# Performance work log

Measured on AMD Instinct MI355X. Metric: run time of the kernel, lower is better.

## Reference

```python
import jax, jax.numpy as jnp
import numpy as np

Q, B, D = 512, 4, 1024      # qlen, batch, d_model
L, H, DH, DI = 4, 16, 64, 4096  # layers, heads, d_head, d_inner
M = 512                      # mem_len


def setup_inputs() -> dict:
    key = jax.random.key(0)
    ks = jax.random.split(key, 10)
    w = lambda i, shape: jax.random.normal(ks[i], shape, jnp.float32) * 0.02
    return dict(
        x=jax.random.normal(ks[0], (Q, B, D), jnp.float32),
        mems=jax.random.normal(ks[1], (L, M, B, D), jnp.float32),
        u=w(2, (H, DH)),
        v=w(3, (H, DH)),
        W_qkv=w(4, (L, D, 3 * H * DH)),
        W_o=w(5, (L, H * DH, D)),
        W_r=w(6, (L, D, H * DH)),
        ln1_g=jnp.ones((L, D), jnp.float32),
        ln1_b=jnp.zeros((L, D), jnp.float32),
        W1=w(7, (L, D, DI)),
        b1=jnp.zeros((L, DI), jnp.float32),
        W2=w(8, (L, DI, D)),
        b2=jnp.zeros((L, D), jnp.float32),
        ln2_g=jnp.ones((L, D), jnp.float32),
        ln2_b=jnp.zeros((L, D), jnp.float32),
    )


def _layer_norm(x, g, b):
    mu = x.mean(-1, keepdims=True)
    var = ((x - mu) ** 2).mean(-1, keepdims=True)
    return (x - mu) * jax.lax.rsqrt(var + 1e-5) * g + b


def _rel_shift(x):
    # x: [q, k, b, n] -> Transformer-XL relative shift
    q, k, b, n = x.shape
    x = jnp.pad(x, ((0, 0), (1, 0), (0, 0), (0, 0)))
    return x.reshape(k + 1, q, b, n)[1:].reshape(q, k, b, n)


def _pos_emb(klen, d):
    pos = jnp.arange(klen - 1, -1, -1.0, dtype=jnp.float32)
    inv_freq = 1.0 / (10000.0 ** (jnp.arange(0, d, 2, dtype=jnp.float32) / d))
    ang = pos[:, None] * inv_freq[None, :]
    return jnp.concatenate([jnp.sin(ang), jnp.cos(ang)], axis=-1)  # [klen, d]


def reference(x, mems, u, v, W_qkv, W_o, W_r, ln1_g, ln1_b, W1, b1, W2, b2, ln2_g, ln2_b):
    q_len, bsz, d = x.shape
    mlen = mems.shape[1]
    klen = mlen + q_len
    r = _pos_emb(klen, d)                       # [klen, d]
    scale = 1.0 / np.sqrt(DH)
    # causal mask with memory: query i may attend key j iff j - i <= mlen
    mask = (jnp.arange(klen)[None, :] - jnp.arange(q_len)[:, None]) > mlen  # [q, k]
    h = x
    for i in range(L):
        cat = jnp.concatenate([mems[i], h], axis=0)       # [klen, b, d]
        heads = cat @ W_qkv[i]                            # [klen, b, 3*H*DH]
        qh, kh, vh = jnp.split(heads, 3, axis=-1)
        qh = qh[-q_len:].reshape(q_len, bsz, H, DH)
        kh = kh.reshape(klen, bsz, H, DH)
        vh = vh.reshape(klen, bsz, H, DH)
        rk = (r @ W_r[i]).reshape(klen, H, DH)            # [klen, H, DH]
        AC = jnp.einsum('ibnd,jbnd->ijbn', qh + u, kh)
        BD = _rel_shift(jnp.einsum('ibnd,jnd->ijbn', qh + v, rk))
        score = (AC + BD) * scale                         # [q, k, b, n]
        score = jnp.where(mask[:, :, None, None], -1e30, score)
        attn = jax.nn.softmax(score, axis=1)
        av = jnp.einsum('ijbn,jbnd->ibnd', attn, vh).reshape(q_len, bsz, H * DH)
        h = _layer_norm(h + av @ W_o[i], ln1_g[i], ln1_b[i])
        ff = jax.nn.relu(h @ W1[i] + b1[i]) @ W2[i] + b2[i]
        h = _layer_norm(h + ff, ln2_g[i], ln2_b[i])
    return h  # [qlen, bsz, d_model]
```

## Files before the change

kernel.cpp:

```cpp
#include <hip/hip_runtime.h>
#include <hip/hip_bf16.h>
#include <cstdint>

#define QL      512
#define BS      4
#define DMODEL  1024
#define NL      4
#define NH      16
#define DHEAD   64
#define DINNER  4096
#define MLEN    512
#define KLEN_   1024
#define HD_     1024
#define THD     3072
#define ROWS_H   2048

typedef __attribute__((ext_vector_type(8))) __bf16 bf16x8;
typedef __attribute__((ext_vector_type(4))) __bf16 bf16x4;
typedef __attribute__((ext_vector_type(4))) float  f32x4;

enum EpiMode { EPI_F32 = 0, EPI_BF16 = 1, EPI_RELU_BF16 = 2 };

__device__ __forceinline__ void glds16(const void* g, void* l) {
  __builtin_amdgcn_global_load_lds(
      (const __attribute__((address_space(1))) unsigned int*)g,
      (__attribute__((address_space(3))) unsigned int*)l, 16, 0, 0);
}

template<int BM, int BN, int WMT, int WNT, int EPI>
__global__ __launch_bounds__(256) void gemm_bt(
    const __bf16* __restrict__ A, const __bf16* __restrict__ Bt,
    void* __restrict__ Cv, const float* __restrict__ bias,
    int K, int lda, int ldb, int ldc,
    long sA, long Bn, long Cn)
{
  constexpr int WCOLS = BN / (WNT * 16);
  constexpr int WROWS = BM / (WMT * 16);
  static_assert(WCOLS * WROWS == 4, "must be 4 waves");
  __shared__ __align__(16) char smem[(BM + BN) * 64];
  char* sAm = smem;
  char* sBm = smem + BM * 64;

  const int bz = blockIdx.z;
  A  += (size_t)bz * sA;
  Bt += (size_t)bz * Bn;
  const size_t coff = (size_t)bz * Cn;

  const int tid  = threadIdx.x;
  const int wave = tid >> 6, lane = tid & 63;
  const int quad = lane >> 4, mrow = lane & 15;
  const int wr = wave / WCOLS, wc = wave % WCOLS;
  const int bm0 = blockIdx.x * BM, bn0 = blockIdx.y * BN;

  const int srow = lane >> 2;
  const int skq  = (lane & 3) ^ (srow & 3);
  const __bf16* gA = A  + (size_t)(bm0 + wave * (BM / 64) * 16 + srow) * lda + skq * 8;
  const __bf16* gB = Bt + (size_t)(bn0 + wave * (BN / 64) * 16 + srow) * ldb + skq * 8;
  char* lA = sAm + wave * (BM / 64) * 1024;
  char* lB = sBm + wave * (BN / 64) * 1024;

  const int aswz = (quad ^ (mrow & 3)) << 4;

  const f32x4 zero = {0.f, 0.f, 0.f, 0.f};
  f32x4 acc[WMT][WNT];
#pragma unroll
  for (int a = 0; a < WMT; ++a)
#pragma unroll
    for (int b = 0; b < WNT; ++b) acc[a][b] = zero;

  for (int k0 = 0; k0 < K; k0 += 32) {
#pragma unroll
    for (int p = 0; p < BM / 64; ++p)
      glds16(gA + (size_t)p * 16 * lda + k0, lA + p * 1024);
#pragma unroll
    for (int p = 0; p < BN / 64; ++p)
      glds16(gB + (size_t)p * 16 * ldb + k0, lB + p * 1024);
    __syncthreads();
    bf16x8 afr[WMT], bfr[WNT];
#pragma unroll
    for (int mt = 0; mt < WMT; ++mt)
      afr[mt] = *(const bf16x8*)(sAm + (wr * (WMT * 16) + mt * 16 + mrow) * 64 + aswz);
#pragma unroll
    for (int nt = 0; nt < WNT; ++nt)
      bfr[nt] = *(const bf16x8*)(sBm + (wc * (WNT * 16) + nt * 16 + mrow) * 64 + aswz);
#pragma unroll
    for (int mt = 0; mt < WMT; ++mt)
#pragma unroll
      for (int nt = 0; nt < WNT; ++nt)
        acc[mt][nt] = __builtin_amdgcn_mfma_f32_16x16x32_bf16(afr[mt], bfr[nt], acc[mt][nt], 0, 0, 0);
    __syncthreads();
  }

#pragma unroll
  for (int mt = 0; mt < WMT; ++mt) {
#pragma unroll
    for (int nt = 0; nt < WNT; ++nt) {
#pragma unroll
      for (int rr = 0; rr < 4; ++rr) {
        int gm = bm0 + wr * (WMT * 16) + mt * 16 + quad * 4 + rr;
        int gn = bn0 + wc * (WNT * 16) + nt * 16 + mrow;
        float val = acc[mt][nt][rr];
        if constexpr (EPI == EPI_F32) {
          ((float*)Cv)[coff + (size_t)gm * ldc + gn] = val;
        } else if constexpr (EPI == EPI_BF16) {
          ((__bf16*)Cv)[coff + (size_t)gm * ldc + gn] = (__bf16)val;
        } else {
          val += bias[gn];
          ((__bf16*)Cv)[coff + (size_t)gm * ldc + gn] = (__bf16)fmaxf(val, 0.f);
        }
      }
    }
  }
}

__global__ __launch_bounds__(256) void flash_attn(
    const __bf16* __restrict__ qu,
    const __bf16* __restrict__ qv,
    const __bf16* __restrict__ heads,
    const __bf16* __restrict__ rk,
    const __bf16* __restrict__ vt,
    __bf16* __restrict__ avp,
    float* __restrict__ mlpart)
{
  __shared__ __align__(16) char kh_t[64 * 144];
  __shared__ __align__(16) char rv_t[64 * 144];
  __shared__ float raw[64 * 132];

  const int wgid = blockIdx.x;
  const int xcd  = wgid & 7;
  const int slotw = wgid >> 3;
  const int bn   = ((slotw >> 4) << 3) + xcd;
  const int inner = slotw & 15;
  const int t    = inner & 7;
  const int z    = inner >> 3;
  const int i0   = t * 64;
  const int b    = bn >> 4, n = bn & 15;
  const int nt   = t + 9;
  const int h    = (nt + 1) >> 1;
  const int ks   = z ? h : 0;
  const int ke   = z ? nt : h;

  const int tid = threadIdx.x;
  const int wave = tid >> 6, lane = tid & 63;
  const int quad = lane >> 4, mrow = lane & 15;
  const f32x4 zero = {0.f, 0.f, 0.f, 0.f};

  const __bf16* qub = qu + (size_t)bn * QL * DHEAD;
  const __bf16* qvb = qv + (size_t)bn * QL * DHEAD;
  const int qrow = i0 + wave * 16 + mrow;
  bf16x8 quf0 = *(const bf16x8*)(qub + (size_t)qrow * 64 + quad * 8);
  bf16x8 quf1 = *(const bf16x8*)(qub + (size_t)qrow * 64 + 32 + quad * 8);
  bf16x8 qvf0 = *(const bf16x8*)(qvb + (size_t)qrow * 64 + quad * 8);
  bf16x8 qvf1 = *(const bf16x8*)(qvb + (size_t)qrow * 64 + 32 + quad * 8);

  f32x4 o[4];
#pragma unroll
  for (int dt = 0; dt < 4; ++dt) o[dt] = zero;
  float m_r[4], l_r[4];
#pragma unroll
  for (int rr = 0; rr < 4; ++rr) { m_r[rr] = -3.0e38f; l_r[rr] = 0.f; }

  const int sr = tid >> 3;
  const int sc = (tid & 7) * 8;

  const int c0 = 448 - i0;
  const int cpre = c0 + 64 * ks;
#pragma unroll
  for (int p = 0; p < 2; ++p) {
    int r = p * 32 + sr;
    bf16x8 vv = *(const bf16x8*)(rk + (size_t)(cpre + r) * HD_ + n * 64 + sc);
    *(bf16x8*)(rv_t + r * 144 + sc * 2) = vv;
  }
  __syncthreads();
  {
    int slotc = ((cpre >> 6) & 1) * 64;
    __builtin_amdgcn_s_setprio(1);
#pragma unroll
    for (int ct = 0; ct < 4; ++ct) {
      bf16x8 b0 = *(const bf16x8*)(rv_t + (ct * 16 + mrow) * 144 + quad * 16);
      bf16x8 b1 = *(const bf16x8*)(rv_t + (ct * 16 + mrow) * 144 + 64 + quad * 16);
      f32x4 r = __builtin_amdgcn_mfma_f32_16x16x32_bf16(qvf0, b0, zero, 0, 0, 0);
      r = __builtin_amdgcn_mfma_f32_16x16x32_bf16(qvf1, b1, r, 0, 0, 0);
#pragma unroll
      for (int rr = 0; rr < 4; ++rr)
        raw[(wave * 16 + quad * 4 + rr) * 132 + slotc + ct * 16 + mrow] = r[rr];
    }
    __builtin_amdgcn_s_setprio(0);
  }
  __syncthreads();

  const int i_base = i0 + wave * 16 + quad * 4;
  for (int k = ks; k < ke; ++k) {
    const int j0 = k * 64;
#pragma unroll
    for (int p = 0; p < 2; ++p) {
      int r = p * 32 + sr;
      bf16x8 kv = *(const bf16x8*)(heads + (size_t)((j0 + r) * BS + b) * THD + HD_ + n * 64 + sc);
      *(bf16x8*)(kh_t + r * 144 + sc * 2) = kv;
    }
    const int c0n = c0 + 64 * (k + 1);
    if (c0n < KLEN_) {
#pragma unroll
      for (int p = 0; p < 2; ++p) {
        int r = p * 32 + sr;
        bf16x8 rv = *(const bf16x8*)(rk + (size_t)(c0n + r) * HD_ + n * 64 + sc);
        *(bf16x8*)(rv_t + r * 144 + sc * 2) = rv;
      }
    }
    __syncthreads();
    __builtin_amdgcn_s_setprio(1);
    if (c0n < KLEN_) {
      int slotc = ((c0n >> 6) & 1) * 64;
#pragma unroll
      for (int ct = 0; ct < 4; ++ct) {
        bf16x8 b0 = *(const bf16x8*)(rv_t + (ct * 16 + mrow) * 144 + quad * 16);
        bf16x8 b1 = *(const bf16x8*)(rv_t + (ct * 16 + mrow) * 144 + 64 + quad * 16);
        f32x4 r = __builtin_amdgcn_mfma_f32_16x16x32_bf16(qvf0, b0, zero, 0, 0, 0);
        r = __builtin_amdgcn_mfma_f32_16x16x32_bf16(qvf1, b1, r, 0, 0, 0);
#pragma unroll
        for (int rr = 0; rr < 4; ++rr)
          raw[(wave * 16 + quad * 4 + rr) * 132 + slotc + ct * 16 + mrow] = r[rr];
      }
    }
    f32x4 s[4];
#pragma unroll
    for (int ct = 0; ct < 4; ++ct) {
      bf16x8 b0 = *(const bf16x8*)(kh_t + (ct * 16 + mrow) * 144 + quad * 16);
      bf16x8 b1 = *(const bf16x8*)(kh_t + (ct * 16 + mrow) * 144 + 64 + quad * 16);
      s[ct] = __builtin_amdgcn_mfma_f32_16x16x32_bf16(quf0, b0, zero, 0, 0, 0);
      s[ct] = __builtin_amdgcn_mfma_f32_16x16x32_bf16(quf1, b1, s[ct], 0, 0, 0);
    }
    __builtin_amdgcn_s_setprio(0);
    __syncthreads();
#pragma unroll
    for (int p = 0; p < 2; ++p) {
      int r = p * 32 + sr;
      bf16x8 vv = *(const bf16x8*)(vt + (size_t)bn * (DHEAD * KLEN_) + (size_t)r * KLEN_ + j0 + sc);
      *(bf16x8*)(rv_t + r * 144 + sc * 2) = vv;
    }
#pragma unroll
    for (int ct = 0; ct < 4; ++ct) {
#pragma unroll
      for (int rr = 0; rr < 4; ++rr) {
        int i = i_base + rr;
        int j = j0 + ct * 16 + mrow;
        float val;
        if (j - i <= MLEN) {
          int c = j - i + (QL - 1);
          int col = ((c >> 6) & 1) * 64 + (c & 63);
          val = (s[ct][rr] + raw[(wave * 16 + quad * 4 + rr) * 132 + col]) * 0.125f;
        } else val = -3.0e38f;
        s[ct][rr] = val;
      }
    }
    float alpha[4];
#pragma unroll
    for (int rr = 0; rr < 4; ++rr) {
      float mx = fmaxf(fmaxf(s[0][rr], s[1][rr]), fmaxf(s[2][rr], s[3][rr]));
#pragma unroll
      for (int off = 1; off < 16; off <<= 1) mx = fmaxf(mx, __shfl_xor(mx, off));
      float m_new = fmaxf(m_r[rr], mx);
      alpha[rr] = __expf(m_r[rr] - m_new);
      m_r[rr] = m_new;
      float rs = 0.f;
#pragma unroll
      for (int ct = 0; ct < 4; ++ct) {
        float pv = __expf(s[ct][rr] - m_new);
        s[ct][rr] = pv;
        rs += pv;
      }
#pragma unroll
      for (int off = 1; off < 16; off <<= 1) rs += __shfl_xor(rs, off);
      l_r[rr] = l_r[rr] * alpha[rr] + rs;
    }
#pragma unroll
    for (int dt = 0; dt < 4; ++dt)
#pragma unroll
      for (int rr = 0; rr < 4; ++rr) o[dt][rr] *= alpha[rr];
#pragma unroll
    for (int ct = 0; ct < 4; ++ct)
#pragma unroll
      for (int rr = 0; rr < 4; ++rr)
        ((__bf16*)kh_t)[(wave * 16 + quad * 4 + rr) * 72 + ct * 16 + mrow] = (__bf16)s[ct][rr];
    __syncthreads();
    {
      bf16x8 pf0 = *(const bf16x8*)(kh_t + (wave * 16 + mrow) * 144 + quad * 16);
      bf16x8 pf1 = *(const bf16x8*)(kh_t + (wave * 16 + mrow) * 144 + 64 + quad * 16);
      __builtin_amdgcn_s_setprio(1);
#pragma unroll
      for (int dt = 0; dt < 4; ++dt) {
        bf16x8 vf0 = *(const bf16x8*)(rv_t + (dt * 16 + mrow) * 144 + quad * 16);
        bf16x8 vf1 = *(const bf16x8*)(rv_t + (dt * 16 + mrow) * 144 + 64 + quad * 16);
        o[dt] = __builtin_amdgcn_mfma_f32_16x16x32_bf16(pf0, vf0, o[dt], 0, 0, 0);
        o[dt] = __builtin_amdgcn_mfma_f32_16x16x32_bf16(pf1, vf1, o[dt], 0, 0, 0);
      }
      __builtin_amdgcn_s_setprio(0);
    }
    __syncthreads();
  }

  const size_t prow = ((size_t)z * 64 + bn) * 512;
#pragma unroll
  for (int rr = 0; rr < 4; ++rr) {
    int i = i_base + rr;
    float inv = 1.0f / l_r[rr];
#pragma unroll
    for (int dt = 0; dt < 4; ++dt)
      avp[(prow + i) * 64 + dt * 16 + mrow] = (__bf16)(o[dt][rr] * inv);
  }
  if (mrow == 0) {
#pragma unroll
    for (int rr = 0; rr < 4; ++rr) {
      int i = i_base + rr;
      mlpart[(prow + i) * 2]     = m_r[rr];
      mlpart[(prow + i) * 2 + 1] = l_r[rr];
    }
  }
}

__global__ __launch_bounds__(256) void attn_combine(
    const __bf16* __restrict__ avp, const float* __restrict__ mlpart,
    __bf16* __restrict__ av)
{
  int idx = blockIdx.x * 256 + threadIdx.x;
  int dq = idx & 15;
  int i  = (idx >> 4) & 511;
  int bn = idx >> 13;
  int b = bn >> 4, n = bn & 15;
  size_t r0 = (size_t)bn * 512 + i;
  size_t r1 = r0 + (size_t)64 * 512;
  float m1 = mlpart[r0 * 2], l1 = mlpart[r0 * 2 + 1];
  float m2 = mlpart[r1 * 2], l2 = mlpart[r1 * 2 + 1];
  float m  = fmaxf(m1, m2);
  float w1 = l1 * __expf(m1 - m), w2 = l2 * __expf(m2 - m);
  float inv = 1.0f / (w1 + w2);
  w1 *= inv; w2 *= inv;
  bf16x4 o1 = *(const bf16x4*)(avp + r0 * 64 + dq * 4);
  bf16x4 o2 = *(const bf16x4*)(avp + r1 * 64 + dq * 4);
  bf16x4 ov;
#pragma unroll
  for (int j = 0; j < 4; ++j)
    ov[j] = (__bf16)((float)o1[j] * w1 + (float)o2[j] * w2);
  *(bf16x4*)(av + ((size_t)i * BS + b) * HD_ + n * 64 + dq * 4) = ov;
}


__global__ __launch_bounds__(256) void transpose_f32_bf16(
    const float* __restrict__ in, unsigned short* __restrict__ out, int R, int C)
{
  __shared__ float tile[64][66];
  int c0 = blockIdx.x * 64, r0 = blockIdx.y * 64;
  int tx = threadIdx.x, ty = threadIdx.y;
#pragma unroll
  for (int s = 0; s < 8; ++s) {
    int r = ty + s * 8;
    const float* p = in + (size_t)(r0 + r) * C + c0 + 2 * tx;
    tile[r][2 * tx]     = p[0];
    tile[r][2 * tx + 1] = p[1];
  }
  __syncthreads();
#pragma unroll
  for (int s = 0; s < 8; ++s) {
    int c = ty + s * 8;
    __bf16 lo = (__bf16)tile[2 * tx][c];
    __bf16 hi = (__bf16)tile[2 * tx + 1][c];
    unsigned int w = (unsigned int)*(unsigned short*)&lo |
                     ((unsigned int)*(unsigned short*)&hi << 16);
    *(unsigned int*)(out + (size_t)(c0 + c) * R + r0 + 2 * tx) = w;
  }
}

__global__ __launch_bounds__(256) void cast_f32_bf16(const float* __restrict__ in,
                                                     __bf16* __restrict__ out, int n)
{
  int i = blockIdx.x * 256 + threadIdx.x;
  if (i < n) out[i] = (__bf16)in[i];
}

__global__ __launch_bounds__(256) void posemb_kernel(__bf16* __restrict__ r)
{
  int idx = blockIdx.x * 256 + threadIdx.x;
  int p = idx >> 10, c = idx & 1023;
  int t = c & 511;
  float invf = __expf(-((float)t / 512.0f) * 9.210340371976184f);
  float ang = (float)(KLEN_ - 1 - p) * invf;
  float val = (c < 512) ? sinf(ang) : cosf(ang);
  r[idx] = (__bf16)val;
}

__global__ __launch_bounds__(256) void init_h(const float* __restrict__ x,
                                              float* __restrict__ hm,
                                              __bf16* __restrict__ hbf, int n)
{
  int i = blockIdx.x * 256 + threadIdx.x;
  if (i < n) { float t = x[i]; hm[i] = t; hbf[i] = (__bf16)t; }
}

__global__ __launch_bounds__(256) void build_quqv(const __bf16* __restrict__ heads,
                                                  const float* __restrict__ u,
                                                  const float* __restrict__ v,
                                                  __bf16* __restrict__ qu,
                                                  __bf16* __restrict__ qv)
{
  int idx = blockIdx.x * 256 + threadIdx.x;
  int d = idx & 63;
  int i = (idx >> 6) & (QL - 1);
  int bn = idx >> 15;
  int b = bn >> 4, n = bn & 15;
  float q = (float)heads[(size_t)((MLEN + i) * BS + b) * THD + n * 64 + d];
  int ud = n * 64 + d;
  qu[idx] = (__bf16)(q + u[ud]);
  qv[idx] = (__bf16)(q + v[ud]);
}

__global__ __launch_bounds__(256) void build_vt(const unsigned short* __restrict__ heads,
                                                unsigned short* __restrict__ vt)
{
  __shared__ unsigned short tile[64][65];
  int bn = blockIdx.y; int b = bn >> 4, n = bn & 15;
  int j0 = blockIdx.x * 64;
  int tx = threadIdx.x, ty = threadIdx.y;
#pragma unroll
  for (int s = 0; s < 16; ++s) {
    int j = ty + s * 4;
    tile[j][tx] = heads[(size_t)((j0 + j) * BS + b) * THD + 2048 + n * 64 + tx];
  }
  __syncthreads();
#pragma unroll
  for (int s = 0; s < 16; ++s) {
    int d = ty + s * 4;
    vt[(size_t)bn * DHEAD * KLEN_ + (size_t)d * KLEN_ + j0 + tx] = tile[tx][d];
  }
}

__global__ __launch_bounds__(256) void ln_kernel(float* __restrict__ hm,
                                                 const float* __restrict__ d0,
                                                 const float* __restrict__ d1,
                                                 const float* __restrict__ bias,
                                                 const float* __restrict__ g,
                                                 const float* __restrict__ b,
                                                 __bf16* __restrict__ hbf,
                                                 float* __restrict__ outf)
{
  int row = blockIdx.x;
  size_t base = (size_t)row * DMODEL;
  int tid = threadIdx.x;
  float x[4]; float sum = 0.f, sq = 0.f;
#pragma unroll
  for (int p = 0; p < 4; ++p) {
    int c = p * 256 + tid;
    float t = hm[base + c] + d0[base + c];
    if (d1) t += d1[base + c];
    if (bias) t += bias[c];
    x[p] = t; sum += t; sq += t * t;
  }
#pragma unroll
  for (int off = 32; off > 0; off >>= 1) { sum += __shfl_xor(sum, off); sq += __shfl_xor(sq, off); }
  __shared__ float rs[4], rq[4];
  int wave = tid >> 6, lane = tid & 63;
  if (lane == 0) { rs[wave] = sum; rq[wave] = sq; }
  __syncthreads();
  sum = rs[0] + rs[1] + rs[2] + rs[3];
  sq  = rq[0] + rq[1] + rq[2] + rq[3];
  float mu  = sum * (1.0f / DMODEL);
  float var = sq * (1.0f / DMODEL) - mu * mu;
  float rstd = rsqrtf(var + 1e-5f);
#pragma unroll
  for (int p = 0; p < 4; ++p) {
    int c = p * 256 + tid;
    float y = (x[p] - mu) * rstd * g[c] + b[c];
    hm[base + c] = y;
    hbf[base + c] = (__bf16)y;
    if (outf) outf[base + c] = y;
  }
}

extern "C" void kernel_launch(void* const* d_in, const int* in_sizes, int n_in,
                              void* d_out, int out_size, void* d_ws, size_t ws_size,
                              hipStream_t stream) {
  (void)in_sizes; (void)n_in; (void)out_size; (void)ws_size;
  const float* x    = (const float*)d_in[0];
  const float* mems = (const float*)d_in[1];
  const float* u    = (const float*)d_in[2];
  const float* v    = (const float*)d_in[3];
  const float* Wqkv = (const float*)d_in[4];
  const float* Wo   = (const float*)d_in[5];
  const float* Wr   = (const float*)d_in[6];
  const float* ln1g = (const float*)d_in[7];
  const float* ln1b = (const float*)d_in[8];
  const float* W1   = (const float*)d_in[9];
  const float* b1   = (const float*)d_in[10];
  const float* W2   = (const float*)d_in[11];
  const float* b2   = (const float*)d_in[12];
  const float* ln2g = (const float*)d_in[13];
  const float* ln2b = (const float*)d_in[14];

  size_t off = 0;
  char* ws = (char*)d_ws;
  auto alloc = [&](size_t bytes) { size_t o = off; off += (bytes + 255) & ~(size_t)255; return o; };
  __bf16* wT    = (__bf16*)(ws + alloc((size_t)DINNER * DMODEL * 2));
  char*   R1    = (char*)(ws + alloc((size_t)(2 * ROWS_H) * THD * 2));
  __bf16* heads = (__bf16*)R1;
  float*  proj  = (float*)R1;
  __bf16* ff1   = (__bf16*)(R1 + (size_t)ROWS_H * DMODEL * 4);
  __bf16* catb  = (__bf16*)(ws + alloc((size_t)(2 * ROWS_H) * DMODEL * 2));
  __bf16* memsb = catb;
  __bf16* hbf   = catb + (size_t)ROWS_H * DMODEL;
  __bf16* av    = catb;
  float*  mlprt = (float*)hbf;
  __bf16* avp   = wT;
  __bf16* r_bf  = (__bf16*)(ws + alloc((size_t)KLEN_ * DMODEL * 2));
  __bf16* rk4   = (__bf16*)(ws + alloc((size_t)NL * KLEN_ * HD_ * 2));
  __bf16* qu    = (__bf16*)(ws + alloc((size_t)2 * BS * NH * QL * DHEAD * 2));
  __bf16* qv    = qu + (size_t)BS * NH * QL * DHEAD;
  float*  ff2p  = (float*)qu;
  __bf16* vt    = (__bf16*)(ws + alloc((size_t)BS * NH * DHEAD * KLEN_ * 2));
  float*  hm    = (float*)(ws + alloc((size_t)ROWS_H * DMODEL * 4));

  posemb_kernel<<<(KLEN_ * DMODEL) / 256, 256, 0, stream>>>(r_bf);
  init_h<<<(ROWS_H * DMODEL) / 256, 256, 0, stream>>>(x, hm, hbf, ROWS_H * DMODEL);

  for (int i = 0; i < NL; ++i)
    transpose_f32_bf16<<<dim3(HD_ / 64, DMODEL / 64), dim3(32, 8), 0, stream>>>(
        Wr + (size_t)i * DMODEL * HD_, (unsigned short*)(wT + (size_t)i * HD_ * DMODEL),
        DMODEL, HD_);
  gemm_bt<128, 128, 4, 4, EPI_BF16><<<dim3(8, 8, NL), 256, 0, stream>>>(
      r_bf, wT, rk4, nullptr, DMODEL, DMODEL, DMODEL, HD_,
      0, (long)HD_ * DMODEL, (long)KLEN_ * HD_);

  for (int i = 0; i < NL; ++i) {
    cast_f32_bf16<<<(MLEN * BS * DMODEL) / 256, 256, 0, stream>>>(
        mems + (size_t)i * MLEN * BS * DMODEL, memsb, MLEN * BS * DMODEL);
    transpose_f32_bf16<<<dim3(THD / 64, DMODEL / 64), dim3(32, 8), 0, stream>>>(
        Wqkv + (size_t)i * DMODEL * THD, (unsigned short*)wT, DMODEL, THD);
    gemm_bt<128, 128, 4, 4, EPI_BF16><<<dim3(32, 24, 1), 256, 0, stream>>>(
        catb, wT, heads, nullptr, DMODEL, DMODEL, DMODEL, THD, 0, 0, 0);

    build_quqv<<<(BS * NH * QL * DHEAD) / 256, 256, 0, stream>>>(heads, u, v, qu, qv);
    build_vt<<<dim3(KLEN_ / 64, BS * NH), dim3(64, 4), 0, stream>>>(
        (const unsigned short*)heads, (unsigned short*)vt);

    flash_attn<<<dim3(1024), 256, 0, stream>>>(
        qu, qv, heads, rk4 + (size_t)i * KLEN_ * HD_, vt, avp, mlprt);
    attn_combine<<<(64 * 512 * 16) / 256, 256, 0, stream>>>(avp, mlprt, av);

    transpose_f32_bf16<<<dim3(DMODEL / 64, HD_ / 64), dim3(32, 8), 0, stream>>>(
        Wo + (size_t)i * HD_ * DMODEL, (unsigned short*)wT, HD_, DMODEL);
    gemm_bt<128, 64, 4, 2, EPI_F32><<<dim3(16, 16, 1), 256, 0, stream>>>(
        av, wT, proj, nullptr, HD_, HD_, HD_, DMODEL, 0, 0, 0);
    ln_kernel<<<ROWS_H, 256, 0, stream>>>(hm, proj, nullptr, nullptr,
                                          ln1g + i * DMODEL, ln1b + i * DMODEL, hbf, nullptr);

    transpose_f32_bf16<<<dim3(DINNER / 64, DMODEL / 64), dim3(32, 8), 0, stream>>>(
        W1 + (size_t)i * DMODEL * DINNER, (unsigned short*)wT, DMODEL, DINNER);
    gemm_bt<128, 128, 4, 4, EPI_RELU_BF16><<<dim3(16, 32, 1), 256, 0, stream>>>(
        hbf, wT, ff1, b1 + i * DINNER, DMODEL, DMODEL, DMODEL, DINNER, 0, 0, 0);

    transpose_f32_bf16<<<dim3(DMODEL / 64, DINNER / 64), dim3(32, 8), 0, stream>>>(
        W2 + (size_t)i * DINNER * DMODEL, (unsigned short*)wT, DINNER, DMODEL);
    gemm_bt<128, 64, 4, 2, EPI_F32><<<dim3(16, 16, 2), 256, 0, stream>>>(
        ff1, wT, proj, nullptr, DINNER / 2, DINNER, DINNER, DMODEL,
        (long)(DINNER / 2), (long)(DINNER / 2), (long)(ff2p - proj));
    ln_kernel<<<ROWS_H, 256, 0, stream>>>(hm, proj, ff2p, b2 + i * DMODEL,
                                          ln2g + i * DMODEL, ln2b + i * DMODEL, hbf,
                                          (i == NL - 1) ? (float*)d_out : nullptr);
  }
}
```

Before: 1.228 ms.

## Prefetch K/R/V tiles into registers and use exp2 softmax in flash attention

The flash attention loop now loads the next iteration's K and R tiles and the current V tile into registers ahead of time, then writes them to LDS after the barriers. Global load latency should overlap with the MFMA and softmax work instead of stalling before each sync. Softmax moves to base-2 by folding log2(e) into the score scale and using exp2f, including in the combine kernel. The tile-to-workgroup order is reversed so the longer query tiles are scheduled first. In exchange, register pressure rises and occupancy may drop.

```diff
diff --git a/kernel.cpp b/kernel.cpp
--- a/kernel.cpp
+++ b/kernel.cpp
@@ -1,6 +1,7 @@
 #include <hip/hip_runtime.h>
 #include <hip/hip_bf16.h>
 #include <cstdint>
+#include <cmath>
 
 #define QL      512
 #define BS      4
@@ -20,6 +21,8 @@
 typedef __attribute__((ext_vector_type(4))) float  f32x4;
 
 enum EpiMode { EPI_F32 = 0, EPI_BF16 = 1, EPI_RELU_BF16 = 2 };
+
+#define SCL 0.18033688011112042f
 
 __device__ __forceinline__ void glds16(const void* g, void* l) {
   __builtin_amdgcn_global_load_lds(
@@ -131,7 +134,7 @@
   const int slotw = wgid >> 3;
   const int bn   = ((slotw >> 4) << 3) + xcd;
   const int inner = slotw & 15;
-  const int t    = inner & 7;
+  const int t    = 7 - (inner & 7);
   const int z    = inner >> 3;
   const int i0   = t * 64;
   const int b    = bn >> 4, n = bn & 15;
@@ -163,6 +166,8 @@
   const int sr = tid >> 3;
   const int sc = (tid & 7) * 8;
 
+  const __bf16* vtb = vt + (size_t)bn * (DHEAD * KLEN_);
+
   const int c0 = 448 - i0;
   const int cpre = c0 + 64 * ks;
 #pragma unroll
@@ -187,30 +192,35 @@
     }
     __builtin_amdgcn_s_setprio(0);
   }
+  bf16x8 kreg0, kreg1, rreg0, rreg1, vreg0, vreg1;
+  {
+    int j0 = ks * 64;
+    kreg0 = *(const bf16x8*)(heads + (size_t)((j0 + sr) * BS + b) * THD + HD_ + n * 64 + sc);
+    kreg1 = *(const bf16x8*)(heads + (size_t)((j0 + 32 + sr) * BS + b) * THD + HD_ + n * 64 + sc);
+    int c1 = c0 + 64 * (ks + 1);
+    if (c1 < KLEN_) {
+      rreg0 = *(const bf16x8*)(rk + (size_t)(c1 + sr) * HD_ + n * 64 + sc);
+      rreg1 = *(const bf16x8*)(rk + (size_t)(c1 + 32 + sr) * HD_ + n * 64 + sc);
+    }
+  }
   __syncthreads();
 
   const int i_base = i0 + wave * 16 + quad * 4;
   for (int k = ks; k < ke; ++k) {
     const int j0 = k * 64;
-#pragma unroll
-    for (int p = 0; p < 2; ++p) {
-      int r = p * 32 + sr;
-      bf16x8 kv = *(const bf16x8*)(heads + (size_t)((j0 + r) * BS + b) * THD + HD_ + n * 64 + sc);
-      *(bf16x8*)(kh_t + r * 144 + sc * 2) = kv;
-    }
-    const int c0n = c0 + 64 * (k + 1);
-    if (c0n < KLEN_) {
-#pragma unroll
-      for (int p = 0; p < 2; ++p) {
-        int r = p * 32 + sr;
-        bf16x8 rv = *(const bf16x8*)(rk + (size_t)(c0n + r) * HD_ + n * 64 + sc);
-        *(bf16x8*)(rv_t + r * 144 + sc * 2) = rv;
-      }
+    const int cw = c0 + 64 * (k + 1);
+    vreg0 = *(const bf16x8*)(vtb + (size_t)sr * KLEN_ + j0 + sc);
+    vreg1 = *(const bf16x8*)(vtb + (size_t)(32 + sr) * KLEN_ + j0 + sc);
+    *(bf16x8*)(kh_t + sr * 144 + sc * 2) = kreg0;
+    *(bf16x8*)(kh_t + (32 + sr) * 144 + sc * 2) = kreg1;
+    if (cw < KLEN_) {
+      *(bf16x8*)(rv_t + sr * 144 + sc * 2) = rreg0;
+      *(bf16x8*)(rv_t + (32 + sr) * 144 + sc * 2) = rreg1;
     }
     __syncthreads();
     __builtin_amdgcn_s_setprio(1);
-    if (c0n < KLEN_) {
-      int slotc = ((c0n >> 6) & 1) * 64;
+    if (cw < KLEN_) {
+      int slotc = ((cw >> 6) & 1) * 64;
 #pragma unroll
       for (int ct = 0; ct < 4; ++ct) {
         bf16x8 b0 = *(const bf16x8*)(rv_t + (ct * 16 + mrow) * 144 + quad * 16);
@@ -232,12 +242,18 @@
     }
     __builtin_amdgcn_s_setprio(0);
     __syncthreads();
-#pragma unroll
-    for (int p = 0; p < 2; ++p) {
-      int r = p * 32 + sr;
-      bf16x8 vv = *(const bf16x8*)(vt + (size_t)bn * (DHEAD * KLEN_) + (size_t)r * KLEN_ + j0 + sc);
-      *(bf16x8*)(rv_t + r * 144 + sc * 2) = vv;
-    }
+    if (k + 1 < ke) {
+      int j1 = (k + 1) * 64;
+      kreg0 = *(const bf16x8*)(heads + (size_t)((j1 + sr) * BS + b) * THD + HD_ + n * 64 + sc);
+      kreg1 = *(const bf16x8*)(heads + (size_t)((j1 + 32 + sr) * BS + b) * THD + HD_ + n * 64 + sc);
+      int cn2 = c0 + 64 * (k + 2);
+      if (cn2 < KLEN_) {
+        rreg0 = *(const bf16x8*)(rk + (size_t)(cn2 + sr) * HD_ + n * 64 + sc);
+        rreg1 = *(const bf16x8*)(rk + (size_t)(cn2 + 32 + sr) * HD_ + n * 64 + sc);
+      }
+    }
+    *(bf16x8*)(rv_t + sr * 144 + sc * 2) = vreg0;
+    *(bf16x8*)(rv_t + (32 + sr) * 144 + sc * 2) = vreg1;
 #pragma unroll
     for (int ct = 0; ct < 4; ++ct) {
 #pragma unroll
@@ -248,7 +264,7 @@
         if (j - i <= MLEN) {
           int c = j - i + (QL - 1);
           int col = ((c >> 6) & 1) * 64 + (c & 63);
-          val = (s[ct][rr] + raw[(wave * 16 + quad * 4 + rr) * 132 + col]) * 0.125f;
+          val = (s[ct][rr] + raw[(wave * 16 + quad * 4 + rr) * 132 + col]) * SCL;
         } else val = -3.0e38f;
         s[ct][rr] = val;
       }
@@ -260,12 +276,12 @@
 #pragma unroll
       for (int off = 1; off < 16; off <<= 1) mx = fmaxf(mx, __shfl_xor(mx, off));
       float m_new = fmaxf(m_r[rr], mx);
-      alpha[rr] = __expf(m_r[rr] - m_new);
+      alpha[rr] = exp2f(m_r[rr] - m_new);
       m_r[rr] = m_new;
       float rs = 0.f;
 #pragma unroll
       for (int ct = 0; ct < 4; ++ct) {
-        float pv = __expf(s[ct][rr] - m_new);
+        float pv = exp2f(s[ct][rr] - m_new);
         s[ct][rr] = pv;
         rs += pv;
       }
@@ -332,7 +348,7 @@
   float m1 = mlpart[r0 * 2], l1 = mlpart[r0 * 2 + 1];
   float m2 = mlpart[r1 * 2], l2 = mlpart[r1 * 2 + 1];
   float m  = fmaxf(m1, m2);
-  float w1 = l1 * __expf(m1 - m), w2 = l2 * __expf(m2 - m);
+  float w1 = l1 * exp2f(m1 - m), w2 = l2 * exp2f(m2 - m);
   float inv = 1.0f / (w1 + w2);
   w1 *= inv; w2 *= inv;
   bf16x4 o1 = *(const bf16x4*)(avp + r0 * 64 + dq * 4);
```

Measured after the change: 1.235 ms. Within noise of the previous version (+0.6%).
